# Optimization experiments

Hardware: AMD Instinct MI355X
Metric: run time of the kernel (lower is better)

## Reference

```python
import jax, jax.numpy as jnp
import numpy as np

H = 2048  # hidden_size
B = 32    # hardcoded batch in module
T = 4     # sequence length per sample
F = 19    # LSTM input features


def setup_inputs() -> dict:
    key = jax.random.key(0)
    ks = jax.random.split(key, 14)
    s = 0.02
    def n(k, shape, scale=s):
        return jax.random.normal(k, shape, jnp.float32) * scale
    return {
        "state": jax.random.normal(ks[0], (B, T, 15), jnp.float32),
        "action": jax.random.normal(ks[1], (B, T, 4), jnp.float32),
        "conv_w": n(ks[2], (1,), 1.0),
        "conv_b": n(ks[3], (1,), 1.0),
        "w_ih0": n(ks[4], (4 * H, F)),
        "w_hh0": n(ks[5], (4 * H, H)),
        "b_ih0": n(ks[6], (4 * H,)),
        "b_hh0": n(ks[7], (4 * H,)),
        "w_ih1": n(ks[8], (4 * H, H)),
        "w_hh1": n(ks[9], (4 * H, H)),
        "b_ih1": n(ks[10], (4 * H,)),
        "b_hh1": n(ks[11], (4 * H,)),
        "lin_w": n(ks[12], (1, 4 * H)),
        "lin_b": n(ks[13], (1,)),
    }


def lstm_layer(x, w_ih, w_hh, b_ih, b_hh):
    # x: (T, B, in). PyTorch gate order: i, f, g, o. Zero initial state.
    Bn = x.shape[1]
    Hn = w_hh.shape[1]
    h0 = jnp.zeros((Bn, Hn), x.dtype)
    c0 = jnp.zeros((Bn, Hn), x.dtype)
    bias = b_ih + b_hh

    def step(carry, xt):
        h, c = carry
        g = xt @ w_ih.T + h @ w_hh.T + bias  # (B, 4H)
        i, f, gg, o = jnp.split(g, 4, axis=-1)
        c = jax.nn.sigmoid(f) * c + jax.nn.sigmoid(i) * jnp.tanh(gg)
        h = jax.nn.sigmoid(o) * jnp.tanh(c)
        return (h, c), h

    _, ys = jax.lax.scan(step, (h0, c0), x)
    return ys  # (T, B, H)


def reference(state, action, conv_w, conv_b, w_ih0, w_hh0, b_ih0, b_hh0,
              w_ih1, w_hh1, b_ih1, b_hh1, lin_w, lin_b):
    x = jnp.concatenate((state, action), axis=2)       # (B, T, 19)
    # Conv1d(1->1, k=1) on (T,1,19) is a scalar affine; tanh activation.
    x = jnp.tanh(conv_w[0] * x + conv_b[0])            # (B, T, 19)
    # Batch all 32 independent per-sample LSTM calls into one batched LSTM.
    x = jnp.transpose(x, (1, 0, 2))                    # (T, B, 19)
    h = lstm_layer(x, w_ih0, w_hh0, b_ih0, b_hh0)      # (T, B, H)
    h = lstm_layer(h, w_ih1, w_hh1, b_ih1, b_hh1)      # (T, B, H)
    h = jnp.transpose(h, (1, 0, 2)).reshape(B, T * H)  # (32, 4H) sample-major, matches torch reshape
    return jax.nn.sigmoid(h @ lin_w.T + lin_b)         # (32, 1)
```

## Files before the change

### kernel.cpp

```cpp
#include <hip/hip_runtime.h>
#include <hip/hip_bf16.h>
#include <math.h>

typedef __bf16 bf16_t;
typedef bf16_t bf16x8 __attribute__((ext_vector_type(8)));
typedef bf16_t bf16x4 __attribute__((ext_vector_type(4)));
typedef float  f32x4  __attribute__((ext_vector_type(4)));
typedef float  vf4    __attribute__((ext_vector_type(4)));

#define HH 2048
#define BB 32
#define TT 4
#define FF 19
#define NBLK 256
#define NTHR 512

#define LDS_WHH   0
#define LDS_X     131072
#define LDS_WIH0  141312
#define LDS_B0    143872
#define LDS_B1    144000
#define LDS_GP    144128
#define LDS_RED   152576
#define LDS_TOTAL 152608

#define WS_BAR    0
#define BAR_BYTES 16384
#define WS_H0     16384
#define WS_H1     540672
#define WS_G1     1064960

__device__ __forceinline__ float sigm(float x) { return 1.0f / (1.0f + expf(-x)); }

__device__ __forceinline__ void gbar_arrive(char* barbase, int slot, int blk) {
    __syncthreads();
    if (threadIdx.x == 0) {
        unsigned* base = (unsigned*)(barbase + slot * 1024);
        if (__hip_atomic_fetch_add(base + (blk & 7) * 16, 1u, __ATOMIC_RELAXED, __HIP_MEMORY_SCOPE_AGENT) == 31u)
            if (__hip_atomic_fetch_add(base + 128, 1u, __ATOMIC_RELAXED, __HIP_MEMORY_SCOPE_AGENT) == 7u)
                __hip_atomic_store(base + 144, 1u, __ATOMIC_RELAXED, __HIP_MEMORY_SCOPE_AGENT);
    }
}
__device__ __forceinline__ void gbar_wait(char* barbase, int slot) {
    if (threadIdx.x == 0) {
        unsigned* flag = (unsigned*)(barbase + slot * 1024) + 144;
        while (__hip_atomic_load(flag, __ATOMIC_RELAXED, __HIP_MEMORY_SCOPE_AGENT) == 0u)
            __builtin_amdgcn_s_sleep(1);
    }
    __syncthreads();
}

__device__ __forceinline__ float touch2(const float* __restrict__ w, int blk, int r0, int tid) {
    float acc = 0.f;
    #pragma unroll
    for (int rg = 0; rg < 2; ++rg) {
        const float* p = w + ((size_t)((r0 + rg) * 2048 + blk * 8)) * 2048;
        #pragma unroll
        for (int j = 0; j < 8; ++j) {
            vf4 v = *reinterpret_cast<const vf4*>(p + j * 2048 + tid * 4);
            acc += v[0] + v[1] + v[2] + v[3];
        }
    }
    return acc;
}

__device__ __forceinline__ void load_w_lds(char* smem, const float* __restrict__ w, int blk, int tid) {
    char* dst = smem + LDS_WHH;
    #pragma unroll 1
    for (int base = 0; base < 32; base += 8) {
        vf4 v[8];
        #pragma unroll
        for (int j = 0; j < 8; ++j) {
            int row = base + j;
            int gr = (row >> 3) * 2048 + blk * 8 + (row & 7);
            v[j] = *reinterpret_cast<const vf4*>(w + (size_t)gr * 2048 + tid * 4);
        }
        #pragma unroll
        for (int j = 0; j < 8; ++j) {
            int row = base + j;
            bf16x4 bv;
            bv[0] = (bf16_t)v[j][0]; bv[1] = (bf16_t)v[j][1];
            bv[2] = (bf16_t)v[j][2]; bv[3] = (bf16_t)v[j][3];
            unsigned byte = (unsigned)(row * 4096) + (((unsigned)(tid * 8)) ^ (((unsigned)(row & 7)) << 4));
            *reinterpret_cast<bf16x4*>(dst + byte) = bv;
        }
    }
}

__device__ __forceinline__ void step_gemm(const __hip_bfloat16* __restrict__ hprev,
                                          const char* smem, float* gparts,
                                          int lane, int wv, int do_mfma) {
    const int q  = wv >> 1;
    const int kh = wv & 1;
    const int mt = q >> 1, nt = q & 1;
    const int r = lane & 15, g4 = lane >> 4;
    f32x4 acc0 = {0.f,0.f,0.f,0.f}, acc1 = {0.f,0.f,0.f,0.f};
    if (do_mfma) {
        const char* bbase = smem + LDS_WHH;
        const int n = nt * 16 + r;
        const unsigned brow = (unsigned)(n * 4096);
        const unsigned bsw = ((unsigned)(n & 7)) << 4;
        const __hip_bfloat16* aptr = hprev + (mt * 16 + r) * 2048 + g4 * 8;
        const int k0 = kh * 32;
        #pragma unroll
        for (int ks = 0; ks < 32; ks += 2) {
            int ka = k0 + ks, kb = k0 + ks + 1;
            bf16x8 a0 = *reinterpret_cast<const bf16x8*>(aptr + ka * 32);
            bf16x8 b0 = *reinterpret_cast<const bf16x8*>(bbase + brow + (((unsigned)(ka * 64 + g4 * 16)) ^ bsw));
            acc0 = __builtin_amdgcn_mfma_f32_16x16x32_bf16(a0, b0, acc0, 0, 0, 0);
            bf16x8 a1 = *reinterpret_cast<const bf16x8*>(aptr + kb * 32);
            bf16x8 b1 = *reinterpret_cast<const bf16x8*>(bbase + brow + (((unsigned)(kb * 64 + g4 * 16)) ^ bsw));
            acc1 = __builtin_amdgcn_mfma_f32_16x16x32_bf16(a1, b1, acc1, 0, 0, 0);
        }
    }
    f32x4 s = acc0 + acc1;
    #pragma unroll
    for (int r2 = 0; r2 < 4; ++r2)
        gparts[(kh * 32 + mt * 16 + g4 * 4 + r2) * 33 + nt * 16 + r] = s[r2];
}

__device__ __forceinline__ void store_h(__hip_bfloat16* p, float x) {
    __hip_bfloat16 hv = __float2bfloat16(x);
    unsigned short bits = *reinterpret_cast<unsigned short*>(&hv);
    __hip_atomic_store((unsigned short*)p, bits, __ATOMIC_RELAXED, __HIP_MEMORY_SCOPE_AGENT);
}

__global__ __launch_bounds__(NTHR, 2) void fused_lstm(
    const float* __restrict__ state, const float* __restrict__ action,
    const float* __restrict__ conv_w, const float* __restrict__ conv_b,
    const float* __restrict__ w_ih0, const float* __restrict__ w_hh0,
    const float* __restrict__ b_ih0, const float* __restrict__ b_hh0,
    const float* __restrict__ w_ih1, const float* __restrict__ w_hh1,
    const float* __restrict__ b_ih1, const float* __restrict__ b_hh1,
    const float* __restrict__ lin_w, const float* __restrict__ lin_b,
    float* __restrict__ out, char* __restrict__ ws)
{
    extern __shared__ char smem[];
    float* x_lds    = (float*)(smem + LDS_X);
    float* wih0_lds = (float*)(smem + LDS_WIH0);
    float* b0_lds   = (float*)(smem + LDS_B0);
    float* b1_lds   = (float*)(smem + LDS_B1);
    float* gparts   = (float*)(smem + LDS_GP);
    float* red      = (float*)(smem + LDS_RED);

    const int tid  = threadIdx.x;
    const int blk  = blockIdx.x;
    const int lane = tid & 63;
    const int wv   = tid >> 6;
    const int m    = tid >> 3;
    const int u    = tid & 7;

    __hip_bfloat16* h0_ws = (__hip_bfloat16*)(ws + WS_H0);
    __hip_bfloat16* h1_ws = (__hip_bfloat16*)(ws + WS_H1);
    float*          g1    = (float*)(ws + WS_G1);

    float tacc = 0.f;

    {
        float cw = conv_w[0], cb = conv_b[0];
        for (int i = tid; i < TT * BB * FF; i += NTHR) {
            int f = i % FF; int tb = i / FF; int t = tb >> 5; int mm = tb & 31;
            float v = (f < 15) ? state[(mm * TT + t) * 15 + f] : action[(mm * TT + t) * 4 + (f - 15)];
            x_lds[tb * 20 + f] = tanhf(cw * v + cb);
        }
        for (int i = tid; i < 32 * FF; i += NTHR) {
            int n = i / FF; int f = i % FF;
            int gr = (n >> 3) * 2048 + blk * 8 + (n & 7);
            wih0_lds[n * 20 + f] = w_ih0[(size_t)gr * FF + f];
        }
        if (tid < 32) {
            int gr = (tid >> 3) * 2048 + blk * 8 + (tid & 7);
            b0_lds[tid] = b_ih0[gr] + b_hh0[gr];
        }
    }
    load_w_lds(smem, w_hh0, blk, tid);
    __syncthreads();

    float c0 = 0.f;
    for (int t = 0; t < TT; ++t) {
        const __hip_bfloat16* hp = h0_ws + (size_t)((t > 0 ? t - 1 : 0) * BB * HH);
        step_gemm(hp, smem, gparts, lane, wv, t > 0);
        __syncthreads();
        if (tid < 256) {
            float gv[4];
            #pragma unroll
            for (int gate = 0; gate < 4; ++gate) {
                int n = gate * 8 + u;
                float a = gparts[m * 33 + n] + gparts[(32 + m) * 33 + n] + b0_lds[n];
                const float* xr = &x_lds[(t * 32 + m) * 20];
                const float* wr = &wih0_lds[n * 20];
                #pragma unroll
                for (int f = 0; f < FF; ++f) a += xr[f] * wr[f];
                gv[gate] = a;
            }
            float ig = sigm(gv[0]), fg = sigm(gv[1]), g2 = tanhf(gv[2]), og = sigm(gv[3]);
            c0 = fg * c0 + ig * g2;
            store_h(h0_ws + (size_t)(t * 32 + m) * 2048 + blk * 8 + u, og * tanhf(c0));
        }
        gbar_arrive(ws, t, blk);
        tacc += touch2((t < 2) ? w_ih1 : w_hh1, blk, (t & 1) * 2, tid);
        gbar_wait(ws, t);
    }
    if (tacc == 1.2345e30f) ((float*)(ws + 15 * 1024))[tid] = tacc;

    load_w_lds(smem, w_ih1, blk, tid);
    if (tid < 32) {
        int gr = (tid >> 3) * 2048 + blk * 8 + (tid & 7);
        b1_lds[tid] = b_ih1[gr] + b_hh1[gr];
    }
    __syncthreads();
    {
        const int r = lane & 15, g4 = lane >> 4;
        const char* bbase = smem + LDS_WHH;
        const unsigned bsw0 = ((unsigned)(r & 7)) << 4;
        const int mt = wv;
        f32x4 acc0 = {0.f,0.f,0.f,0.f}, acc1 = {0.f,0.f,0.f,0.f};
        const __hip_bfloat16* aptr = h0_ws + (size_t)(mt * 16 + r) * 2048 + g4 * 8;
        #pragma unroll 4
        for (int ks = 0; ks < 64; ++ks) {
            bf16x8 a  = *reinterpret_cast<const bf16x8*>(aptr + ks * 32);
            bf16x8 b0 = *reinterpret_cast<const bf16x8*>(bbase + (unsigned)(r * 4096)        + (((unsigned)(ks * 64 + g4 * 16)) ^ bsw0));
            bf16x8 b1 = *reinterpret_cast<const bf16x8*>(bbase + (unsigned)((16 + r) * 4096) + (((unsigned)(ks * 64 + g4 * 16)) ^ bsw0));
            acc0 = __builtin_amdgcn_mfma_f32_16x16x32_bf16(a, b0, acc0, 0, 0, 0);
            acc1 = __builtin_amdgcn_mfma_f32_16x16x32_bf16(a, b1, acc1, 0, 0, 0);
        }
        #pragma unroll
        for (int r2 = 0; r2 < 4; ++r2) {
            int tb = mt * 16 + g4 * 4 + r2;
            g1[((size_t)tb * 256 + blk) * 32 + r]      = acc0[r2] + b1_lds[r];
            g1[((size_t)tb * 256 + blk) * 32 + 16 + r] = acc1[r2] + b1_lds[16 + r];
        }
    }
    __syncthreads();
    load_w_lds(smem, w_hh1, blk, tid);
    __syncthreads();

    float c1 = 0.f;
    for (int t = 0; t < TT; ++t) {
        const __hip_bfloat16* hp = h1_ws + (size_t)((t > 0 ? t - 1 : 0) * BB * HH);
        step_gemm(hp, smem, gparts, lane, wv, t > 0);
        __syncthreads();
        if (tid < 256) {
            float gv[4];
            #pragma unroll
            for (int gate = 0; gate < 4; ++gate) {
                int n = gate * 8 + u;
                gv[gate] = gparts[m * 33 + n] + gparts[(32 + m) * 33 + n]
                         + g1[((size_t)(t * 32 + m) * 256 + blk) * 32 + n];
            }
            float ig = sigm(gv[0]), fg = sigm(gv[1]), g2 = tanhf(gv[2]), og = sigm(gv[3]);
            c1 = fg * c1 + ig * g2;
            store_h(h1_ws + (size_t)(t * 32 + m) * 2048 + blk * 8 + u, og * tanhf(c1));
        }
        gbar_arrive(ws, 4 + t, blk);
        gbar_wait(ws, 4 + t);
    }

    if (blk < BB) {
        float part = 0.f;
        for (int i = tid; i < 1024; i += NTHR) {
            int k = i * 8; int t = k >> 11; int uu = k & 2047;
            uint4 hv = *reinterpret_cast<const uint4*>(h1_ws + (size_t)(t * 32 + blk) * 2048 + uu);
            const float* lw = lin_w + k;
            #pragma unroll
            for (int j = 0; j < 4; ++j) {
                unsigned wj = (&hv.x)[j];
                float lo = __uint_as_float(wj << 16);
                float hi = __uint_as_float(wj & 0xffff0000u);
                part += lo * lw[2 * j] + hi * lw[2 * j + 1];
            }
        }
        #pragma unroll
        for (int off = 32; off; off >>= 1) part += __shfl_down(part, off, 64);
        if (lane == 0) red[wv] = part;
        __syncthreads();
        if (tid == 0) {
            float s = red[0] + red[1] + red[2] + red[3] + red[4] + red[5] + red[6] + red[7] + lin_b[0];
            out[blk] = 1.f / (1.f + expf(-s));
        }
    }
}

extern "C" void kernel_launch(void* const* d_in, const int* in_sizes, int n_in,
                              void* d_out, int out_size, void* d_ws, size_t ws_size,
                              hipStream_t stream) {
    const float* state  = (const float*)d_in[0];
    const float* action = (const float*)d_in[1];
    const float* conv_w = (const float*)d_in[2];
    const float* conv_b = (const float*)d_in[3];
    const float* w_ih0  = (const float*)d_in[4];
    const float* w_hh0  = (const float*)d_in[5];
    const float* b_ih0  = (const float*)d_in[6];
    const float* b_hh0  = (const float*)d_in[7];
    const float* w_ih1  = (const float*)d_in[8];
    const float* w_hh1  = (const float*)d_in[9];
    const float* b_ih1  = (const float*)d_in[10];
    const float* b_hh1  = (const float*)d_in[11];
    const float* lin_w  = (const float*)d_in[12];
    const float* lin_b  = (const float*)d_in[13];
    float* out = (float*)d_out;
    char*  ws  = (char*)d_ws;

    hipMemsetAsync(ws, 0, BAR_BYTES, stream);

    void* args[] = {&state, &action, &conv_w, &conv_b, &w_ih0, &w_hh0, &b_ih0, &b_hh0,
                    &w_ih1, &w_hh1, &b_ih1, &b_hh1, &lin_w, &lin_b, &out, &ws};
    hipLaunchCooperativeKernel((void*)fused_lstm, dim3(NBLK), dim3(NTHR), args,
                               LDS_TOTAL, stream);
}
```

Before: 352.3 us.

## Peel zero-state timestep and overlap weight loads with grid barriers

The first timestep of each LSTM layer is peeled out. With a zero hidden state it needs no recurrent GEMM, so its gates come only from the input projection (layer 0) or the precomputed input GEMM (layer 1). Each layer's recurrent weight load into LDS now runs between the grid-barrier arrive and wait, hiding it behind the barrier latency. The w_ih1 load is likewise moved into the last layer-0 barrier window, and the L2 prefetch touch of upcoming weights is removed. The cooperative launch is replaced with a plain launch, which relies on all 256 blocks being co-resident for the spin barriers to stay correct.

```diff
diff --git a/kernel.cpp b/kernel.cpp
--- a/kernel.cpp
+++ b/kernel.cpp
@@ -25,7 +25,7 @@
 #define LDS_TOTAL 152608
 
 #define WS_BAR    0
-#define BAR_BYTES 16384
+#define BAR_BYTES 8192
 #define WS_H0     16384
 #define WS_H1     540672
 #define WS_G1     1064960
@@ -50,20 +50,6 @@
     __syncthreads();
 }
 
-__device__ __forceinline__ float touch2(const float* __restrict__ w, int blk, int r0, int tid) {
-    float acc = 0.f;
-    #pragma unroll
-    for (int rg = 0; rg < 2; ++rg) {
-        const float* p = w + ((size_t)((r0 + rg) * 2048 + blk * 8)) * 2048;
-        #pragma unroll
-        for (int j = 0; j < 8; ++j) {
-            vf4 v = *reinterpret_cast<const vf4*>(p + j * 2048 + tid * 4);
-            acc += v[0] + v[1] + v[2] + v[3];
-        }
-    }
-    return acc;
-}
-
 __device__ __forceinline__ void load_w_lds(char* smem, const float* __restrict__ w, int blk, int tid) {
     char* dst = smem + LDS_WHH;
     #pragma unroll 1
@@ -89,29 +75,27 @@
 
 __device__ __forceinline__ void step_gemm(const __hip_bfloat16* __restrict__ hprev,
                                           const char* smem, float* gparts,
-                                          int lane, int wv, int do_mfma) {
+                                          int lane, int wv) {
     const int q  = wv >> 1;
     const int kh = wv & 1;
     const int mt = q >> 1, nt = q & 1;
     const int r = lane & 15, g4 = lane >> 4;
     f32x4 acc0 = {0.f,0.f,0.f,0.f}, acc1 = {0.f,0.f,0.f,0.f};
-    if (do_mfma) {
-        const char* bbase = smem + LDS_WHH;
-        const int n = nt * 16 + r;
-        const unsigned brow = (unsigned)(n * 4096);
-        const unsigned bsw = ((unsigned)(n & 7)) << 4;
-        const __hip_bfloat16* aptr = hprev + (mt * 16 + r) * 2048 + g4 * 8;
-        const int k0 = kh * 32;
-        #pragma unroll
-        for (int ks = 0; ks < 32; ks += 2) {
-            int ka = k0 + ks, kb = k0 + ks + 1;
-            bf16x8 a0 = *reinterpret_cast<const bf16x8*>(aptr + ka * 32);
-            bf16x8 b0 = *reinterpret_cast<const bf16x8*>(bbase + brow + (((unsigned)(ka * 64 + g4 * 16)) ^ bsw));
-            acc0 = __builtin_amdgcn_mfma_f32_16x16x32_bf16(a0, b0, acc0, 0, 0, 0);
-            bf16x8 a1 = *reinterpret_cast<const bf16x8*>(aptr + kb * 32);
-            bf16x8 b1 = *reinterpret_cast<const bf16x8*>(bbase + brow + (((unsigned)(kb * 64 + g4 * 16)) ^ bsw));
-            acc1 = __builtin_amdgcn_mfma_f32_16x16x32_bf16(a1, b1, acc1, 0, 0, 0);
-        }
+    const char* bbase = smem + LDS_WHH;
+    const int n = nt * 16 + r;
+    const unsigned brow = (unsigned)(n * 4096);
+    const unsigned bsw = ((unsigned)(n & 7)) << 4;
+    const __hip_bfloat16* aptr = hprev + (mt * 16 + r) * 2048 + g4 * 8;
+    const int k0 = kh * 32;
+    #pragma unroll
+    for (int ks = 0; ks < 32; ks += 2) {
+        int ka = k0 + ks, kb = k0 + ks + 1;
+        bf16x8 a0 = *reinterpret_cast<const bf16x8*>(aptr + ka * 32);
+        bf16x8 b0 = *reinterpret_cast<const bf16x8*>(bbase + brow + (((unsigned)(ka * 64 + g4 * 16)) ^ bsw));
+        acc0 = __builtin_amdgcn_mfma_f32_16x16x32_bf16(a0, b0, acc0, 0, 0, 0);
+        bf16x8 a1 = *reinterpret_cast<const bf16x8*>(aptr + kb * 32);
+        bf16x8 b1 = *reinterpret_cast<const bf16x8*>(bbase + brow + (((unsigned)(kb * 64 + g4 * 16)) ^ bsw));
+        acc1 = __builtin_amdgcn_mfma_f32_16x16x32_bf16(a1, b1, acc1, 0, 0, 0);
     }
     f32x4 s = acc0 + acc1;
     #pragma unroll
@@ -154,8 +138,6 @@
     __hip_bfloat16* h1_ws = (__hip_bfloat16*)(ws + WS_H1);
     float*          g1    = (float*)(ws + WS_G1);
 
-    float tacc = 0.f;
-
     {
         float cw = conv_w[0], cb = conv_b[0];
         for (int i = tid; i < TT * BB * FF; i += NTHR) {
@@ -173,13 +155,31 @@
             b0_lds[tid] = b_ih0[gr] + b_hh0[gr];
         }
     }
+    __syncthreads();
+
+    float c0 = 0.f;
+    if (tid < 256) {
+        float gv[4];
+        #pragma unroll
+        for (int gate = 0; gate < 4; ++gate) {
+            int n = gate * 8 + u;
+            float a = b0_lds[n];
+            const float* xr = &x_lds[m * 20];
+            const float* wr = &wih0_lds[n * 20];
+            #pragma unroll
+            for (int f = 0; f < FF; ++f) a += xr[f] * wr[f];
+            gv[gate] = a;
+        }
+        float ig = sigm(gv[0]), fg = sigm(gv[1]), g2 = tanhf(gv[2]), og = sigm(gv[3]);
+        c0 = fg * c0 + ig * g2;
+        store_h(h0_ws + (size_t)m * 2048 + blk * 8 + u, og * tanhf(c0));
+    }
+    gbar_arrive(ws, 0, blk);
     load_w_lds(smem, w_hh0, blk, tid);
-    __syncthreads();
-
-    float c0 = 0.f;
-    for (int t = 0; t < TT; ++t) {
-        const __hip_bfloat16* hp = h0_ws + (size_t)((t > 0 ? t - 1 : 0) * BB * HH);
-        step_gemm(hp, smem, gparts, lane, wv, t > 0);
+    gbar_wait(ws, 0);
+
+    for (int t = 1; t < TT; ++t) {
+        step_gemm(h0_ws + (size_t)(t - 1) * BB * HH, smem, gparts, lane, wv);
         __syncthreads();
         if (tid < 256) {
             float gv[4];
@@ -198,17 +198,16 @@
             store_h(h0_ws + (size_t)(t * 32 + m) * 2048 + blk * 8 + u, og * tanhf(c0));
         }
         gbar_arrive(ws, t, blk);
-        tacc += touch2((t < 2) ? w_ih1 : w_hh1, blk, (t & 1) * 2, tid);
+        if (t == 3) {
+            load_w_lds(smem, w_ih1, blk, tid);
+            if (tid < 32) {
+                int gr = (tid >> 3) * 2048 + blk * 8 + (tid & 7);
+                b1_lds[tid] = b_ih1[gr] + b_hh1[gr];
+            }
+        }
         gbar_wait(ws, t);
     }
-    if (tacc == 1.2345e30f) ((float*)(ws + 15 * 1024))[tid] = tacc;
-
-    load_w_lds(smem, w_ih1, blk, tid);
-    if (tid < 32) {
-        int gr = (tid >> 3) * 2048 + blk * 8 + (tid & 7);
-        b1_lds[tid] = b_ih1[gr] + b_hh1[gr];
-    }
-    __syncthreads();
+
     {
         const int r = lane & 15, g4 = lane >> 4;
         const char* bbase = smem + LDS_WHH;
@@ -232,13 +231,25 @@
         }
     }
     __syncthreads();
+
+    float c1 = 0.f;
+    if (tid < 256) {
+        float gv[4];
+        #pragma unroll
+        for (int gate = 0; gate < 4; ++gate) {
+            int n = gate * 8 + u;
+            gv[gate] = g1[((size_t)m * 256 + blk) * 32 + n];
+        }
+        float ig = sigm(gv[0]), fg = sigm(gv[1]), g2 = tanhf(gv[2]), og = sigm(gv[3]);
+        c1 = fg * c1 + ig * g2;
+        store_h(h1_ws + (size_t)m * 2048 + blk * 8 + u, og * tanhf(c1));
+    }
+    gbar_arrive(ws, 4, blk);
     load_w_lds(smem, w_hh1, blk, tid);
-    __syncthreads();
-
-    float c1 = 0.f;
-    for (int t = 0; t < TT; ++t) {
-        const __hip_bfloat16* hp = h1_ws + (size_t)((t > 0 ? t - 1 : 0) * BB * HH);
-        step_gemm(hp, smem, gparts, lane, wv, t > 0);
+    gbar_wait(ws, 4);
+
+    for (int t = 1; t < TT; ++t) {
+        step_gemm(h1_ws + (size_t)(t - 1) * BB * HH, smem, gparts, lane, wv);
         __syncthreads();
         if (tid < 256) {
             float gv[4];
@@ -303,8 +314,7 @@
 
     hipMemsetAsync(ws, 0, BAR_BYTES, stream);
 
-    void* args[] = {&state, &action, &conv_w, &conv_b, &w_ih0, &w_hh0, &b_ih0, &b_hh0,
-                    &w_ih1, &w_hh1, &b_ih1, &b_hh1, &lin_w, &lin_b, &out, &ws};
-    hipLaunchCooperativeKernel((void*)fused_lstm, dim3(NBLK), dim3(NTHR), args,
-                               LDS_TOTAL, stream);
-}
+    hipLaunchKernelGGL(fused_lstm, dim3(NBLK), dim3(NTHR), LDS_TOTAL, stream,
+                       state, action, conv_w, conv_b, w_ih0, w_hh0, b_ih0, b_hh0,
+                       w_ih1, w_hh1, b_ih1, b_hh1, lin_w, lin_b, out, ws);
+}
```

Result: faster. 297.5 us (-15.6%).
